# Optimization experiments

Hardware: AMD Instinct MI355X
Metric: run time of the kernel (lower is better)

## Reference

```python
import jax, jax.numpy as jnp
import numpy as np

# ---- fixed kernels (match kornia.filters.canny defaults) ----
_POS = [(1, 2), (2, 2), (2, 1), (2, 0), (1, 0), (0, 0), (0, 1), (0, 2)]  # 8 directions, 45deg steps
_nms = np.zeros((8, 1, 3, 3), np.float32)
_hyst = np.zeros((8, 1, 3, 3), np.float32)
for _i, (_r, _c) in enumerate(_POS):
    _nms[_i, 0, 1, 1] = 1.0
    _nms[_i, 0, _r, _c] = -1.0
    _hyst[_i, 0, _r, _c] = 1.0
NMS_K = jnp.asarray(_nms)
HYST_K = jnp.asarray(_hyst)
SOBEL_X = jnp.asarray(np.array([[-1, 0, 1], [-2, 0, 2], [-1, 0, 1]], np.float32).reshape(1, 1, 3, 3))
SOBEL_Y = jnp.asarray(np.array([[-1, -2, -1], [0, 0, 0], [1, 2, 1]], np.float32).reshape(1, 1, 3, 3))


def _conv(x, w, pad):
    return jax.lax.conv_general_dilated(x, w, (1, 1), [(pad, pad), (pad, pad)],
                                        dimension_numbers=('NCHW', 'OIHW', 'NCHW'))


def _gauss_blur(x):
    # 5x5 gaussian, sigma=1, reflect padding (kornia gaussian_blur2d defaults)
    t = jnp.arange(5, dtype=x.dtype) - 2.0
    g = jnp.exp(-0.5 * t * t)
    g = g / g.sum()
    xp = jnp.pad(x, ((0, 0), (0, 0), (2, 2), (2, 2)), mode='reflect')
    x = _conv(xp, g.reshape(1, 1, 5, 1), 0)
    return _conv(x, g.reshape(1, 1, 1, 5), 0)


def canny_edges(img, low=0.1, high=0.2, eps=1e-6):
    # img: (N, 1, H, W) grayscale stack
    b = _gauss_blur(img)
    bp = jnp.pad(b, ((0, 0), (0, 0), (1, 1), (1, 1)), mode='edge')  # replicate pad for sobel
    gx = _conv(bp, SOBEL_X, 0)
    gy = _conv(bp, SOBEL_Y, 0)
    mag = jnp.sqrt(gx * gx + gy * gy + eps)                  # (N,1,H,W)
    ang = jnp.round(jnp.arctan2(gy, gx) * (180.0 / np.pi) / 45.0)  # in {-4..4}
    # angle-dependent non-max suppression via 8 directional difference kernels
    nmsv = _conv(mag, NMS_K, 1)                               # (N,8,H,W)
    pos = jnp.mod(ang, 8).astype(jnp.int32)
    neg = jnp.mod(ang + 4, 8).astype(jnp.int32)
    sp = jnp.take_along_axis(nmsv, pos, axis=1)
    sn = jnp.take_along_axis(nmsv, neg, axis=1)
    mag = mag * (jnp.minimum(sp, sn) > 0.0)
    # double threshold: weak=0.5, strong=1.0
    edges = (mag > low).astype(mag.dtype) * 0.5 + (mag > high) * 0.5

    # hysteresis: iterate until fixed point (weak pixels touching strong become strong)
    def cond(c):
        return ~jnp.all(c[0] == c[1])

    def body(c):
        e, _ = c
        weak = (e == 0.5).astype(e.dtype)
        strong = (e == 1.0).astype(e.dtype)
        hm = jnp.any(_conv(e, HYST_K, 1) == 1.0, axis=1, keepdims=True).astype(e.dtype)
        hm = hm * weak + strong
        return hm + (hm == 0) * weak * 0.5, e

    edges, _ = jax.lax.while_loop(cond, body, (edges, -jnp.ones_like(edges)))
    return edges


def setup_inputs() -> dict:
    key = jax.random.key(0)
    k1, k2 = jax.random.split(key)
    x = jax.random.normal(k1, (1, 64, 512, 512), dtype=jnp.float32)
    params = jnp.ones((1,), dtype=jnp.int64)
    indices = jax.random.randint(k2, (32,), 0, 64, dtype=jnp.int64)
    return {'x': x, 'params': params, 'indices': indices}


def reference(x, params, indices):
    if int(params[0]) == 0:
        return x
    sel = jnp.transpose(x, (1, 0, 2, 3))[indices]        # (K, 1, H, W)
    tf = canny_edges(sel)                                 # (K, 1, H, W) in {0, 0.5, 1}
    return x[:, indices] * jnp.transpose(tf, (1, 0, 2, 3))
```

## Files before the change

### kernel.cpp

```cpp
#include <hip/hip_runtime.h>
#include <cstdint>
#include <math.h>



constexpr int HH = 512;
constexpr int WW = 512;
constexpr int HW = HH * WW;
constexpr int KCH = 32;
constexpr int WORDS = HW / 32;

constexpr int TD = 32;
constexpr int NT = HH / TD;

constexpr int IN_D = 40;
constexpr int VP_R = 36, VP_C = 40;
constexpr int BL_D = 36;
constexpr int SQ_D = 34;

constexpr double E2 = 0.13533528323661269189;
constexpr double E1 = 0.60653065971263342360;
constexpr double GS = ((((E2 + E1) + 1.0) + E1) + E2);
constexpr double GW0 = E2 / GS, GW1 = E1 / GS, GW2 = 1.0 / GS;

constexpr double T1 = 0.4142135623730950488;
constexpr double T2 = 2.4142135623730950488;

constexpr double SQ_HI = 0.2 * 0.2;
constexpr double SQ_LO = 0.1 * 0.1;

__device__ __forceinline__ int reflect_idx(int v) {
    return v < 0 ? -v : (v > 511 ? 1022 - v : v);
}
__device__ __forceinline__ int clampi(int v) {
    return v < 0 ? 0 : (v > 511 ? 511 : v);
}

__device__ const int AY1[4] = {0, 1, 1, 1};
__device__ const int AX1[4] = {1, 1, 0, -1};

__global__ __launch_bounds__(256) void canny_fused(const float* __restrict__ x,
                                                   const int* __restrict__ idx,
                                                   unsigned int* __restrict__ weakb,
                                                   unsigned int* __restrict__ strongb) {
    __shared__ __align__(16) char lds[23296];
    double* vp_s = (double*)lds;
    double* sq_s = (double*)lds;
    float*  in_s = (float*)(lds + 11520);
    double* bl_s = (double*)(lds + 11520);
    unsigned char* ax_s = (unsigned char*)(lds + 21888);
    unsigned char* RUm = (unsigned char*)(lds + 22912);
    unsigned char* RDm = RUm + 34;
    unsigned char* CLm = RUm + 68;
    unsigned char* CRm = RUm + 102;
    unsigned short* rmap = (unsigned short*)(lds + 23048);
    unsigned short* cmap = rmap + 40;

    int tile = blockIdx.x;
    int k = tile >> 8;
    int t = tile & 255;
    int ty0 = (t >> 4) * TD;
    int tx0 = (t & 15) * TD;
    int tid = threadIdx.x;

    int ch = idx[k];
    const float* img = x + (size_t)ch * HW;

    if (tid < 40) {
        rmap[tid] = (unsigned short)reflect_idx(ty0 - 4 + tid);
        cmap[tid] = (unsigned short)reflect_idx(tx0 - 4 + tid);
    } else if (tid >= 64 && tid < 98) {
        int am = tid - 64;
        int u = ty0 - 1 + am;
        RUm[am] = (unsigned char)(clampi(u - 1) - (ty0 - 2));
        RDm[am] = (unsigned char)(clampi(u + 1) - (ty0 - 2));
    } else if (tid >= 128 && tid < 162) {
        int bm = tid - 128;
        int v = tx0 - 1 + bm;
        CLm[bm] = (unsigned char)(clampi(v - 1) - (tx0 - 2));
        CRm[bm] = (unsigned char)(clampi(v + 1) - (tx0 - 2));
    }
    __syncthreads();

    {
        int a = tid / 40, b = tid - a * 40;
        while (a < 40) {
            in_s[a * IN_D + b] = img[(int)rmap[a] * WW + (int)cmap[b]];
            b += 16; a += 6;
            if (b >= 40) { b -= 40; a += 1; }
        }
    }
    __syncthreads();

    const double g[5] = {GW0, GW1, GW2, GW1, GW0};

    if (tid < 240) {
        int rg = tid / 40;
        int b  = tid - 40 * rg;
        int a0 = 6 * rg;
        double w[10];
        #pragma unroll
        for (int j = 0; j < 10; j++) w[j] = (double)in_s[(a0 + j) * IN_D + b];
        #pragma unroll
        for (int i = 0; i < 6; i++) {
            double acc = g[0] * w[i];
            acc += g[1] * w[i + 1];
            acc += g[2] * w[i + 2];
            acc += g[3] * w[i + 3];
            acc += g[4] * w[i + 4];
            vp_s[(a0 + i) * VP_C + b] = acc;
        }
    }
    __syncthreads();

    {
        int a = tid / 36, b = tid - 36 * (tid / 36);
        while (a < 36) {
            const double* vr = vp_s + a * VP_C + b;
            double acc = g[0] * vr[0];
            acc += g[1] * vr[1];
            acc += g[2] * vr[2];
            acc += g[3] * vr[3];
            acc += g[4] * vr[4];
            bl_s[a * BL_D + b] = acc;
            b += 4; a += 7;
            if (b >= 36) { b -= 36; a += 1; }
        }
    }
    __syncthreads();

    {
        int am = tid / 34, bm = tid - 34 * am;
        while (am < 34) {
            int ru = RUm[am], r0 = am + 1, rd = RDm[am];
            int cl = CLm[bm], c0 = bm + 1, cr = CRm[bm];
            double v00 = bl_s[ru * BL_D + cl], v01 = bl_s[ru * BL_D + c0], v02 = bl_s[ru * BL_D + cr];
            double v10 = bl_s[r0 * BL_D + cl],                              v12 = bl_s[r0 * BL_D + cr];
            double v20 = bl_s[rd * BL_D + cl], v21 = bl_s[rd * BL_D + c0], v22 = bl_s[rd * BL_D + cr];
            double gxv = ((((-v00 + v02) + (-2.0 * v10)) + (2.0 * v12)) + (-v20)) + v22;
            double gyv = ((((-v00 + (-2.0 * v01)) + (-v02)) + v20) + (2.0 * v21)) + v22;
            sq_s[am * SQ_D + bm] = (gxv * gxv + gyv * gyv) + 1e-6;

            double axv = fabs(gxv), ayv = fabs(gyv);
            int axis;
            if (ayv < T1 * axv) axis = 0;
            else if (ayv > T2 * axv) axis = 2;
            else {
                double gxf = (gyv < 0.0) ? -gxv : gxv;
                axis = (gxf > 0.0) ? 1 : 3;
            }
            if (am >= 1 && am <= TD && bm >= 1 && bm <= TD)
                ax_s[(am - 1) * TD + (bm - 1)] = (unsigned char)axis;

            bm += 18; am += 7;
            if (bm >= 34) { bm -= 34; am += 1; }
        }
    }
    __syncthreads();

    #pragma unroll
    for (int q4 = 0; q4 < TD * TD / 256; q4++) {
        int l = q4 * 256 + tid;
        int oy = l >> 5, ox = l & 31;
        int gy = ty0 + oy, gx = tx0 + ox;

        int axis = ax_s[oy * TD + ox];
        int dy = AY1[axis], dx = AX1[axis];
        double s = sq_s[(oy + 1) * SQ_D + (ox + 1)];

        int y1 = gy + dy, x1 = gx + dx;
        int y2 = gy - dy, x2 = gx - dx;
        double s1 = (y1 >= 0 && y1 < HH && x1 >= 0 && x1 < WW)
                        ? sq_s[(oy + 1 + dy) * SQ_D + (ox + 1 + dx)] : 0.0;
        double s2 = (y2 >= 0 && y2 < HH && x2 >= 0 && x2 < WW)
                        ? sq_s[(oy + 1 - dy) * SQ_D + (ox + 1 - dx)] : 0.0;
        bool keep = (s > s1) && (s > s2);

        bool strong = keep && (s > SQ_HI);
        bool weak = keep && (s > SQ_LO) && !strong;

        unsigned long long wb = __ballot(weak);
        unsigned long long sb = __ballot(strong);
        if ((tid & 31) == 0) {
            unsigned int ww = (tid & 32) ? (unsigned int)(wb >> 32) : (unsigned int)wb;
            unsigned int sw = (tid & 32) ? (unsigned int)(sb >> 32) : (unsigned int)sb;
            size_t w32 = ((size_t)k * HW + (size_t)gy * WW + tx0) >> 5;
            weakb[w32] = ww;
            strongb[w32] = sw;
        }
    }
}

__global__ __launch_bounds__(1024) void hyst_iterate(const unsigned int* __restrict__ weakb,
                                                     unsigned int* __restrict__ strongb) {
    int k = blockIdx.x;
    __shared__ unsigned int Sm[WORDS];
    __shared__ int s_changed;
    int tid = threadIdx.x;

    const unsigned int* wsrc = weakb + (size_t)k * WORDS;
    unsigned int* ssrc = strongb + (size_t)k * WORDS;

    if (tid == 0) s_changed = 0;
    for (int i = tid; i < WORDS; i += 1024) Sm[i] = ssrc[i];
    unsigned int wreg[8];
    #pragma unroll
    for (int q = 0; q < 8; q++) wreg[q] = wsrc[tid * 8 + q];
    __syncthreads();

    for (;;) {
        int loc = 0;
        #pragma unroll
        for (int q = 0; q < 8; q++) {
            int w = tid * 8 + q;
            unsigned int s = Sm[w];
            unsigned int wk = wreg[q] & ~s;
            if (!wk) continue;
            int j = w & 15;
            unsigned int L = j ? Sm[w - 1] : 0u;
            unsigned int R = (j < 15) ? Sm[w + 1] : 0u;
            unsigned int D = (s << 1) | (L >> 31) | (s >> 1) | (R << 31);
            if (w >= 16) {
                unsigned int cu = Sm[w - 16];
                unsigned int Lu = j ? Sm[w - 17] : 0u;
                unsigned int Ru = (j < 15) ? Sm[w - 15] : 0u;
                D |= cu | (cu << 1) | (Lu >> 31) | (cu >> 1) | (Ru << 31);
            }
            if (w < WORDS - 16) {
                unsigned int cd = Sm[w + 16];
                unsigned int Ld = j ? Sm[w + 15] : 0u;
                unsigned int Rd = (j < 15) ? Sm[w + 17] : 0u;
                D |= cd | (cd << 1) | (Ld >> 31) | (cd >> 1) | (Rd << 31);
            }
            unsigned int promoted = wk & D;
            if (promoted) { Sm[w] = s | promoted; loc = 1; }
        }
        if (loc) s_changed = 1;
        __syncthreads();
        int chg = s_changed;
        __syncthreads();
        if (!chg) break;
        if (tid == 0) s_changed = 0;
        __syncthreads();
    }

    for (int i = tid; i < WORDS; i += 1024) ssrc[i] = Sm[i];
}

__global__ void mul_kernel(const float* __restrict__ x,
                           const int* __restrict__ idx,
                           const unsigned int* __restrict__ weakb,
                           const unsigned int* __restrict__ strongb,
                           float* __restrict__ out) {
    int gid = blockIdx.x * blockDim.x + threadIdx.x;
    int p = gid * 4;
    if (p >= KCH * HW) return;
    int k = p >> 18;
    int r = p & (HW - 1);
    int ch = idx[k];

    unsigned int sw = strongb[p >> 5];
    unsigned int ww = weakb[p >> 5];
    int b0 = p & 31;

    const float4 xv = *reinterpret_cast<const float4*>(x + (size_t)ch * HW + r);
    float t[4];
    #pragma unroll
    for (int i = 0; i < 4; i++) {
        int b = b0 + i;
        t[i] = ((sw >> b) & 1u) ? 1.0f : (((ww >> b) & 1u) ? 0.5f : 0.0f);
    }
    float4 o;
    o.x = xv.x * t[0];
    o.y = xv.y * t[1];
    o.z = xv.z * t[2];
    o.w = xv.w * t[3];
    *reinterpret_cast<float4*>(out + (size_t)p) = o;
}

extern "C" void kernel_launch(void* const* d_in, const int* in_sizes, int n_in,
                              void* d_out, int out_size, void* d_ws, size_t ws_size,
                              hipStream_t stream) {
    const float* x = (const float*)d_in[0];
    const int* idx = (const int*)d_in[2];
    float* out = (float*)d_out;

    char* ws = (char*)d_ws;
    unsigned int* weakb = (unsigned int*)ws;
    unsigned int* strongb = (unsigned int*)(ws + 1048576);

    int ntiles = KCH * NT * NT;
    canny_fused<<<ntiles, 256, 0, stream>>>(x, idx, weakb, strongb);
    hyst_iterate<<<KCH, 1024, 0, stream>>>(weakb, strongb);
    mul_kernel<<<(KCH * HW / 4) / 256, 256, 0, stream>>>(x, idx, weakb, strongb, out);
}
```

Before: 67.68 us.

## Compute blur and Sobel in fp32 with fp64 recheck for near-threshold pixels

Switches the Gaussian blur, Sobel and magnitude stages from double to float, halving LDS footprint, and pads the LDS arrays to odd strides. Pixels whose angle bin, NMS comparison or thresholds fall within a small relative margin are flagged and recomputed in double precision from the input tile by a noinline helper, so the output should still match the fp64 path. It also drops the reflect/clamp lookup tables and one barrier. The aim is to cut the cost of fp64 arithmetic and LDS traffic. The risks are divergence when the recheck fires and possible misclassification if a borderline case escapes the margin test.

```diff
diff --git a/kernel.cpp b/kernel.cpp
--- a/kernel.cpp
+++ b/kernel.cpp
@@ -1,7 +1,6 @@
 #include <hip/hip_runtime.h>
 #include <cstdint>
 #include <math.h>
-
 
 
 constexpr int HH = 512;
@@ -13,10 +12,10 @@
 constexpr int TD = 32;
 constexpr int NT = HH / TD;
 
-constexpr int IN_D = 40;
-constexpr int VP_R = 36, VP_C = 40;
-constexpr int BL_D = 36;
-constexpr int SQ_D = 34;
+constexpr int IN_P = 41;
+constexpr int VP_P = 41;
+constexpr int BL_P = 37;
+constexpr int SQ_P = 35;
 
 constexpr double E2 = 0.13533528323661269189;
 constexpr double E1 = 0.60653065971263342360;
@@ -25,7 +24,6 @@
 
 constexpr double T1 = 0.4142135623730950488;
 constexpr double T2 = 2.4142135623730950488;
-
 constexpr double SQ_HI = 0.2 * 0.2;
 constexpr double SQ_LO = 0.1 * 0.1;
 
@@ -38,23 +36,77 @@
 
 __device__ const int AY1[4] = {0, 1, 1, 1};
 __device__ const int AX1[4] = {1, 1, 0, -1};
+
+__device__ __attribute__((noinline))
+void recheck64(const float* in_s, int gy, int gx, int ty0, int tx0,
+               bool& strong, bool& weak) {
+    const double G[5] = {GW0, GW1, GW2, GW1, GW0};
+
+    auto blur64 = [&](int iy, int ix) -> double {
+        double acc = 0.0;
+        #pragma unroll
+        for (int i = 0; i < 5; i++) {
+            double col = 0.0;
+            #pragma unroll
+            for (int j = 0; j < 5; j++)
+                col += G[j] * (double)in_s[(iy - ty0 + 2 + j) * IN_P + (ix - tx0 + 2 + i)];
+            acc += G[i] * col;
+        }
+        return acc;
+    };
+    auto sobel64 = [&](int py, int px, double& gxv, double& gyv) {
+        int ru = clampi(py - 1), r0 = py, rd = clampi(py + 1);
+        int cl = clampi(px - 1), c0 = px, cr = clampi(px + 1);
+        double v00 = blur64(ru, cl), v01 = blur64(ru, c0), v02 = blur64(ru, cr);
+        double v10 = blur64(r0, cl),                        v12 = blur64(r0, cr);
+        double v20 = blur64(rd, cl), v21 = blur64(rd, c0), v22 = blur64(rd, cr);
+        gxv = ((((-v00 + v02) + (-2.0 * v10)) + (2.0 * v12)) + (-v20)) + v22;
+        gyv = ((((-v00 + (-2.0 * v01)) + (-v02)) + v20) + (2.0 * v21)) + v22;
+    };
+
+    double gxc, gyc;
+    sobel64(gy, gx, gxc, gyc);
+    double s = (gxc * gxc + gyc * gyc) + 1e-6;
+
+    double ax = fabs(gxc), ay = fabs(gyc);
+    int axis;
+    if (ay < T1 * ax) axis = 0;
+    else if (ay > T2 * ax) axis = 2;
+    else {
+        double gxf = (gyc < 0.0) ? -gxc : gxc;
+        axis = (gxf > 0.0) ? 1 : 3;
+    }
+    int dy = AY1[axis], dx = AX1[axis];
+
+    double s1 = 0.0, s2 = 0.0, tx, ty;
+    int y1 = gy + dy, x1 = gx + dx, y2 = gy - dy, x2 = gx - dx;
+    if (y1 >= 0 && y1 < HH && x1 >= 0 && x1 < WW) {
+        sobel64(y1, x1, tx, ty);
+        s1 = (tx * tx + ty * ty) + 1e-6;
+    }
+    if (y2 >= 0 && y2 < HH && x2 >= 0 && x2 < WW) {
+        sobel64(y2, x2, tx, ty);
+        s2 = (tx * tx + ty * ty) + 1e-6;
+    }
+    bool keep = (s > s1) && (s > s2);
+    strong = keep && (s > SQ_HI);
+    weak = keep && (s > SQ_LO) && !strong;
+}
 
 __global__ __launch_bounds__(256) void canny_fused(const float* __restrict__ x,
                                                    const int* __restrict__ idx,
                                                    unsigned int* __restrict__ weakb,
                                                    unsigned int* __restrict__ strongb) {
-    __shared__ __align__(16) char lds[23296];
-    double* vp_s = (double*)lds;
-    double* sq_s = (double*)lds;
-    float*  in_s = (float*)(lds + 11520);
-    double* bl_s = (double*)(lds + 11520);
-    unsigned char* ax_s = (unsigned char*)(lds + 21888);
-    unsigned char* RUm = (unsigned char*)(lds + 22912);
+    __shared__ __align__(16) char lds[18960];
+    float* in_s = (float*)lds;
+    float* vp_s = (float*)(lds + 6560);
+    float* sq_s = (float*)(lds + 6560);
+    float* bl_s = (float*)(lds + 12464);
+    unsigned char* ax_s = (unsigned char*)(lds + 17792);
+    unsigned char* RUm = (unsigned char*)(lds + 18816);
     unsigned char* RDm = RUm + 34;
     unsigned char* CLm = RUm + 68;
     unsigned char* CRm = RUm + 102;
-    unsigned short* rmap = (unsigned short*)(lds + 23048);
-    unsigned short* cmap = rmap + 40;
 
     int tile = blockIdx.x;
     int k = tile >> 8;
@@ -66,49 +118,44 @@
     int ch = idx[k];
     const float* img = x + (size_t)ch * HW;
 
-    if (tid < 40) {
-        rmap[tid] = (unsigned short)reflect_idx(ty0 - 4 + tid);
-        cmap[tid] = (unsigned short)reflect_idx(tx0 - 4 + tid);
+    if (tid < 34) {
+        int u = ty0 - 1 + tid;
+        RUm[tid] = (unsigned char)(clampi(u - 1) - (ty0 - 2));
+        RDm[tid] = (unsigned char)(clampi(u + 1) - (ty0 - 2));
     } else if (tid >= 64 && tid < 98) {
-        int am = tid - 64;
-        int u = ty0 - 1 + am;
-        RUm[am] = (unsigned char)(clampi(u - 1) - (ty0 - 2));
-        RDm[am] = (unsigned char)(clampi(u + 1) - (ty0 - 2));
-    } else if (tid >= 128 && tid < 162) {
-        int bm = tid - 128;
+        int bm = tid - 64;
         int v = tx0 - 1 + bm;
         CLm[bm] = (unsigned char)(clampi(v - 1) - (tx0 - 2));
         CRm[bm] = (unsigned char)(clampi(v + 1) - (tx0 - 2));
     }
-    __syncthreads();
 
     {
-        int a = tid / 40, b = tid - a * 40;
+        int a = tid / 40, b = tid - (tid / 40) * 40;
         while (a < 40) {
-            in_s[a * IN_D + b] = img[(int)rmap[a] * WW + (int)cmap[b]];
+            in_s[a * IN_P + b] = img[reflect_idx(ty0 - 4 + a) * WW + reflect_idx(tx0 - 4 + b)];
             b += 16; a += 6;
             if (b >= 40) { b -= 40; a += 1; }
         }
     }
     __syncthreads();
 
-    const double g[5] = {GW0, GW1, GW2, GW1, GW0};
+    const float gf0 = (float)GW0, gf1 = (float)GW1, gf2 = (float)GW2;
 
     if (tid < 240) {
         int rg = tid / 40;
-        int b  = tid - 40 * rg;
+        int b = tid - 40 * rg;
         int a0 = 6 * rg;
-        double w[10];
+        float w[10];
         #pragma unroll
-        for (int j = 0; j < 10; j++) w[j] = (double)in_s[(a0 + j) * IN_D + b];
+        for (int j = 0; j < 10; j++) w[j] = in_s[(a0 + j) * IN_P + b];
         #pragma unroll
         for (int i = 0; i < 6; i++) {
-            double acc = g[0] * w[i];
-            acc += g[1] * w[i + 1];
-            acc += g[2] * w[i + 2];
-            acc += g[3] * w[i + 3];
-            acc += g[4] * w[i + 4];
-            vp_s[(a0 + i) * VP_C + b] = acc;
+            float acc = gf0 * w[i];
+            acc += gf1 * w[i + 1];
+            acc += gf2 * w[i + 2];
+            acc += gf1 * w[i + 3];
+            acc += gf0 * w[i + 4];
+            vp_s[(a0 + i) * VP_P + b] = acc;
         }
     }
     __syncthreads();
@@ -116,42 +163,47 @@
     {
         int a = tid / 36, b = tid - 36 * (tid / 36);
         while (a < 36) {
-            const double* vr = vp_s + a * VP_C + b;
-            double acc = g[0] * vr[0];
-            acc += g[1] * vr[1];
-            acc += g[2] * vr[2];
-            acc += g[3] * vr[3];
-            acc += g[4] * vr[4];
-            bl_s[a * BL_D + b] = acc;
+            const float* vr = vp_s + a * VP_P + b;
+            float acc = gf0 * vr[0];
+            acc += gf1 * vr[1];
+            acc += gf2 * vr[2];
+            acc += gf1 * vr[3];
+            acc += gf0 * vr[4];
+            bl_s[a * BL_P + b] = acc;
             b += 4; a += 7;
             if (b >= 36) { b -= 36; a += 1; }
         }
     }
     __syncthreads();
 
+    const float T1f = (float)T1, T2f = (float)T2;
     {
-        int am = tid / 34, bm = tid - 34 * am;
+        int am = tid / 34, bm = tid - 34 * (tid / 34);
         while (am < 34) {
             int ru = RUm[am], r0 = am + 1, rd = RDm[am];
             int cl = CLm[bm], c0 = bm + 1, cr = CRm[bm];
-            double v00 = bl_s[ru * BL_D + cl], v01 = bl_s[ru * BL_D + c0], v02 = bl_s[ru * BL_D + cr];
-            double v10 = bl_s[r0 * BL_D + cl],                              v12 = bl_s[r0 * BL_D + cr];
-            double v20 = bl_s[rd * BL_D + cl], v21 = bl_s[rd * BL_D + c0], v22 = bl_s[rd * BL_D + cr];
-            double gxv = ((((-v00 + v02) + (-2.0 * v10)) + (2.0 * v12)) + (-v20)) + v22;
-            double gyv = ((((-v00 + (-2.0 * v01)) + (-v02)) + v20) + (2.0 * v21)) + v22;
-            sq_s[am * SQ_D + bm] = (gxv * gxv + gyv * gyv) + 1e-6;
-
-            double axv = fabs(gxv), ayv = fabs(gyv);
-            int axis;
-            if (ayv < T1 * axv) axis = 0;
-            else if (ayv > T2 * axv) axis = 2;
-            else {
-                double gxf = (gyv < 0.0) ? -gxv : gxv;
-                axis = (gxf > 0.0) ? 1 : 3;
+            float v00 = bl_s[ru * BL_P + cl], v01 = bl_s[ru * BL_P + c0], v02 = bl_s[ru * BL_P + cr];
+            float v10 = bl_s[r0 * BL_P + cl],                              v12 = bl_s[r0 * BL_P + cr];
+            float v20 = bl_s[rd * BL_P + cl], v21 = bl_s[rd * BL_P + c0], v22 = bl_s[rd * BL_P + cr];
+            float gxv = ((((-v00 + v02) + (-2.0f * v10)) + (2.0f * v12)) + (-v20)) + v22;
+            float gyv = ((((-v00 + (-2.0f * v01)) + (-v02)) + v20) + (2.0f * v21)) + v22;
+            sq_s[am * SQ_P + bm] = (gxv * gxv + gyv * gyv) + 1e-6f;
+
+            if (am >= 1 && am <= TD && bm >= 1 && bm <= TD) {
+                float axf = fabsf(gxv), ayf = fabsf(gyv);
+                int axis;
+                if (ayf < T1f * axf) axis = 0;
+                else if (ayf > T2f * axf) axis = 2;
+                else {
+                    float gxf = (gyv < 0.0f) ? -gxv : gxv;
+                    axis = (gxf > 0.0f) ? 1 : 3;
+                }
+                float mrg = 1e-4f * (axf + ayf);
+                bool aflag = (fabsf(ayf - T1f * axf) <= mrg) ||
+                             (fabsf(ayf - T2f * axf) <= mrg) ||
+                             (axf <= mrg) || (ayf <= mrg);
+                ax_s[(am - 1) * TD + (bm - 1)] = (unsigned char)(axis | (aflag ? 4 : 0));
             }
-            if (am >= 1 && am <= TD && bm >= 1 && bm <= TD)
-                ax_s[(am - 1) * TD + (bm - 1)] = (unsigned char)axis;
-
             bm += 18; am += 7;
             if (bm >= 34) { bm -= 34; am += 1; }
         }
@@ -164,20 +216,31 @@
         int oy = l >> 5, ox = l & 31;
         int gy = ty0 + oy, gx = tx0 + ox;
 
-        int axis = ax_s[oy * TD + ox];
+        unsigned char av = ax_s[oy * TD + ox];
+        int axis = av & 3;
+        bool flag = (av & 4) != 0;
         int dy = AY1[axis], dx = AX1[axis];
-        double s = sq_s[(oy + 1) * SQ_D + (ox + 1)];
+        float s = sq_s[(oy + 1) * SQ_P + (ox + 1)];
 
         int y1 = gy + dy, x1 = gx + dx;
         int y2 = gy - dy, x2 = gx - dx;
-        double s1 = (y1 >= 0 && y1 < HH && x1 >= 0 && x1 < WW)
-                        ? sq_s[(oy + 1 + dy) * SQ_D + (ox + 1 + dx)] : 0.0;
-        double s2 = (y2 >= 0 && y2 < HH && x2 >= 0 && x2 < WW)
-                        ? sq_s[(oy + 1 - dy) * SQ_D + (ox + 1 - dx)] : 0.0;
+        bool in1 = (y1 >= 0) && (y1 < HH) && (x1 >= 0) && (x1 < WW);
+        bool in2 = (y2 >= 0) && (y2 < HH) && (x2 >= 0) && (x2 < WW);
+        float s1 = in1 ? sq_s[(oy + 1 + dy) * SQ_P + (ox + 1 + dx)] : 0.0f;
+        float s2 = in2 ? sq_s[(oy + 1 - dy) * SQ_P + (ox + 1 - dx)] : 0.0f;
         bool keep = (s > s1) && (s > s2);
-
-        bool strong = keep && (s > SQ_HI);
-        bool weak = keep && (s > SQ_LO) && !strong;
+        bool strong = keep && (s > 0.04f);
+        bool weak = keep && (s > 0.01f) && !strong;
+
+        const float e = 1e-4f;
+        flag = flag || (in1 && fabsf(s - s1) <= e * (s + s1));
+        flag = flag || (in2 && fabsf(s - s2) <= e * (s + s2));
+        flag = flag || (fabsf(s - 0.04f) <= e * (s + 0.04f));
+        flag = flag || (fabsf(s - 0.01f) <= e * (s + 0.01f));
+
+        if (__builtin_expect((int)flag, 0)) {
+            recheck64(in_s, gy, gx, ty0, tx0, strong, weak);
+        }
 
         unsigned long long wb = __ballot(weak);
         unsigned long long sb = __ballot(strong);
```

After: 141.9 us. 2.1x slower.
